# Kernel tuning notes

Measured on AMD Instinct MI355X. Metric: run time of the kernel, lower is better.

The kernel has to match this reference:

```python
import jax, jax.numpy as jnp
import numpy as np

B, N, M, K = 8, 9225, 4096, 32
D = 2          # coordinate dim
HID = 64       # MLP hidden
DOUT = 16      # MLP output / f_y channels


def setup_inputs() -> dict:
    key = jax.random.key(0)
    ks = jax.random.split(key, 10)
    y = jax.random.uniform(ks[0], (B, N, D), dtype=jnp.float32)
    x = jax.random.uniform(ks[1], (B, M, D), dtype=jnp.float32)
    f_y = jax.random.uniform(ks[2], (B, N, DOUT), dtype=jnp.float32)
    weights = jax.random.uniform(ks[3], (B, N), dtype=jnp.float32)
    neighbors_index = jax.random.randint(ks[4], (B, M, K), 0, N, dtype=jnp.int64)
    drop = jax.random.uniform(ks[5], (B, M, K)) < 0.1
    neighbors_index = jnp.where(drop, jnp.int64(-1), neighbors_index)
    # LinearChannelMLP params: 4 -> 64 -> 16, gelu between
    W1 = jax.random.normal(ks[6], (2 * D, HID), dtype=jnp.float32) * (1.0 / np.sqrt(2 * D))
    b1 = jnp.zeros((HID,), dtype=jnp.float32)
    W2 = jax.random.normal(ks[7], (HID, DOUT), dtype=jnp.float32) * (1.0 / np.sqrt(HID))
    b2 = jnp.zeros((DOUT,), dtype=jnp.float32)
    return {"y": y, "x": x, "f_y": f_y, "weights": weights,
            "W1": W1, "b1": b1, "W2": W2, "b2": b2,
            "neighbors_index": neighbors_index}


def _batched_gather(table, idx):
    # table: [B, N, ...], idx: [B, M, K] -> [B, M, K, ...]
    return jax.vmap(lambda t, i: t[i])(table, idx)


def reference(y, x, f_y, weights, W1, b1, W2, b2, neighbors_index):
    idx = jnp.where(neighbors_index == -1, 0, neighbors_index)      # [B,M,K]
    valid = (neighbors_index != -1).astype(y.dtype)[..., None]      # [B,M,K,1]

    rep_y = _batched_gather(y, idx)                                 # [B,M,K,D]
    in_f = _batched_gather(f_y, idx)                                # [B,M,K,DOUT]
    self_x = jnp.broadcast_to(x[:, :, None, :], rep_y.shape)        # [B,M,K,D]

    agg = jnp.concatenate([rep_y, self_x], axis=-1)                 # [B,M,K,2D]
    h = jax.nn.gelu(agg @ W1 + b1, approximate=False)               # [B,M,K,HID]
    kval = h @ W2 + b2                                              # [B,M,K,DOUT]

    kval = kval * in_f                                              # linear transform: k(x,y)*f(y)
    w_nbr = _batched_gather(weights, idx)[..., None]                # [B,M,K,1]
    kval = kval * w_nbr * valid
    return kval.sum(axis=2)                                         # [B,M,DOUT]
```

## Files before the change

kernel.cpp:

```cpp
#include <hip/hip_runtime.h>
#include <hip/hip_bf16.h>

#define B_    8
#define N_    9225
#define M_    4096
#define K_    32
#define HID_  64
#define DOUT_ 16

typedef __attribute__((ext_vector_type(8))) short short8;
typedef __attribute__((ext_vector_type(4))) float floatx4;
typedef __attribute__((ext_vector_type(2))) float f32x2;

static __device__ __forceinline__ short f2bf(float f) {
    __hip_bfloat16 h = __float2bfloat16(f);
    return __builtin_bit_cast(short, h);
}
static __device__ __forceinline__ float bf2f(short s) {
    unsigned u = ((unsigned)(unsigned short)s) << 16;
    return __builtin_bit_cast(float, u);
}
static __device__ __forceinline__ f32x2 splat2(float v) { return (f32x2){v, v}; }

static __device__ __forceinline__ float row16_sum(float v) {
    int t;
    t = __builtin_amdgcn_update_dpp(0, __builtin_bit_cast(int, v), 0x111, 0xF, 0xF, true);
    v += __builtin_bit_cast(float, t);
    t = __builtin_amdgcn_update_dpp(0, __builtin_bit_cast(int, v), 0x112, 0xF, 0xF, true);
    v += __builtin_bit_cast(float, t);
    t = __builtin_amdgcn_update_dpp(0, __builtin_bit_cast(int, v), 0x114, 0xF, 0xF, true);
    v += __builtin_bit_cast(float, t);
    t = __builtin_amdgcn_update_dpp(0, __builtin_bit_cast(int, v), 0x118, 0xF, 0xF, true);
    v += __builtin_bit_cast(float, t);
    return v;
}

static __device__ __forceinline__ f32x2 gelu2(f32x2 x) {
    const f32x2 xsq = x * x;
    const f32x2 t   = __builtin_elementwise_fma(xsq, splat2(0.035677408f), splat2(0.79788456f));
    const f32x2 z   = x * t;
    const f32x2 u   = z * z;
    const f32x2 a   = u + splat2(105.0f);
    const f32x2 nin = __builtin_elementwise_fma(u, a, splat2(945.0f));
    const f32x2 num = z * nin;
    const f32x2 bq  = __builtin_elementwise_fma(u, splat2(15.0f), splat2(420.0f));
    const f32x2 den = __builtin_elementwise_fma(u, bq, splat2(945.0f));
    const f32x2 r   = { __builtin_amdgcn_rcpf(den[0]), __builtin_amdgcn_rcpf(den[1]) };
    f32x2 th = num * r;
    th = __builtin_elementwise_min(__builtin_elementwise_max(th, splat2(-1.0f)), splat2(1.0f));
    const f32x2 hx = x * splat2(0.5f);
    return __builtin_elementwise_fma(hx, th, hx);
}

__global__ __launch_bounds__(256, 4) void it_kernel(
    const float* __restrict__ y,
    const float* __restrict__ x,
    const float* __restrict__ f_y,
    const float* __restrict__ weights,
    const float* __restrict__ W1,
    const float* __restrict__ b1,
    const float* __restrict__ W2,
    const float* __restrict__ b2,
    const int*   __restrict__ nbr,
    float*       __restrict__ out)
{
    __shared__ float b1L[64];
    __shared__ float b2L[16];

    const int tid = threadIdx.x;
    if (tid < 64) b1L[tid] = b1[tid];
    if (tid < 16) b2L[tid] = b2[tid];

    const int lane = tid & 63;
    const int q    = lane >> 4;
    const int nlo  = lane & 15;

    const int blk   = blockIdx.x;
    const int batch = blk & 7;
    const int pblk  = blk >> 3;
    const int wid   = tid >> 6;
    const int row0  = __builtin_amdgcn_readfirstlane(batch * M_ + pblk * 16 + wid * 4);
    const int bbase = batch * N_;

    short8 w1h[4];
    #pragma unroll
    for (int t = 0; t < 4; ++t) {
        #pragma unroll
        for (int jj = 0; jj < 8; ++jj) w1h[t][jj] = 0;
        #pragma unroll
        for (int jj = 0; jj < 4; ++jj) {
            const float wv = W1[jj * HID_ + t * 16 + nlo];
            w1h[t][jj] = (q == 0) ? f2bf(wv) : (short)0;
        }
    }

    short8 w2f[2];
    #pragma unroll
    for (int ch = 0; ch < 2; ++ch)
        #pragma unroll
        for (int jj = 0; jj < 8; ++jj) {
            const int H = (ch * 2 + (jj >> 2)) * 16 + q * 4 + (jj & 3);
            w2f[ch][jj] = f2bf(W2[H * DOUT_ + nlo]);
        }

    short xh[8], xl[8];
    #pragma unroll
    for (int it = 0; it < 4; ++it) {
        const float2 xv = *(const float2*)(x + (size_t)(row0 + it) * 2);
        const short h0 = f2bf(xv.x); const short l0 = f2bf(xv.x - bf2f(h0));
        const short h1 = f2bf(xv.y); const short l1 = f2bf(xv.y - bf2f(h1));
        xh[it * 2] = h0; xh[it * 2 + 1] = h1;
        xl[it * 2] = l0; xl[it * 2 + 1] = l1;
    }

    int raw[8];
    #pragma unroll
    for (int ph = 0; ph < 8; ++ph) {
        const int it = ph >> 1, h = ph & 1;
        raw[ph] = nbr[(size_t)(row0 + it) * K_ + h * 16 + nlo];
    }

    float2 yv[8]; float sw[8]; floatx4 fv[8];
    #define GATH(P) { \
        const int rv  = raw[P]; \
        const int vld = rv >= 0; \
        const int bn  = bbase + (vld ? rv : 0); \
        yv[P] = *(const float2*)(y + (size_t)bn * 2); \
        const float wv_ = weights[bn]; \
        sw[P] = vld ? wv_ : 0.0f; \
        fv[P] = *(const floatx4*)(f_y + (size_t)bn * DOUT_ + q * 4); \
    }
    GATH(0); GATH(1);

    __syncthreads();

    float partial[4] = {0.f, 0.f, 0.f, 0.f};
    #pragma unroll
    for (int ph = 0; ph < 8; ++ph) {
        if (ph + 2 < 8) GATH(ph + 2);
        const int it = ph >> 1;

        const float y0 = yv[ph].x, y1 = yv[ph].y;
        const short yh0 = f2bf(y0); const short yl0 = f2bf(y0 - bf2f(yh0));
        const short yh1 = f2bf(y1); const short yl1 = f2bf(y1 - bf2f(yh1));
        const bool q0 = (q == 0);
        const short z = 0;
        const short8 bhi = { q0 ? yh0 : z, q0 ? yh1 : z,
                             q0 ? xh[it * 2] : z, q0 ? xh[it * 2 + 1] : z,
                             z, z, z, z };
        const short8 blo = { q0 ? yl0 : z, q0 ? yl1 : z,
                             q0 ? xl[it * 2] : z, q0 ? xl[it * 2 + 1] : z,
                             z, z, z, z };

        floatx4 a1[4];
        #pragma unroll
        for (int t = 0; t < 4; ++t) {
            a1[t] = *(const floatx4*)&b1L[t * 16 + q * 4];
            a1[t] = __builtin_amdgcn_mfma_f32_16x16x32_bf16(w1h[t], bhi, a1[t], 0, 0, 0);
            a1[t] = __builtin_amdgcn_mfma_f32_16x16x32_bf16(w1h[t], blo, a1[t], 0, 0, 0);
        }

        short hv[16];
        #pragma unroll
        for (int t = 0; t < 4; ++t) {
            const f32x2 g01 = gelu2((f32x2){a1[t][0], a1[t][1]});
            const f32x2 g23 = gelu2((f32x2){a1[t][2], a1[t][3]});
            hv[t * 4 + 0] = f2bf(g01[0]); hv[t * 4 + 1] = f2bf(g01[1]);
            hv[t * 4 + 2] = f2bf(g23[0]); hv[t * 4 + 3] = f2bf(g23[1]);
        }
        const short8 hf0 = {hv[0], hv[1], hv[2],  hv[3],  hv[4],  hv[5],  hv[6],  hv[7]};
        const short8 hf1 = {hv[8], hv[9], hv[10], hv[11], hv[12], hv[13], hv[14], hv[15]};

        floatx4 acc = *(const floatx4*)&b2L[q * 4];
        acc = __builtin_amdgcn_mfma_f32_16x16x32_bf16(w2f[0], hf0, acc, 0, 0, 0);
        acc = __builtin_amdgcn_mfma_f32_16x16x32_bf16(w2f[1], hf1, acc, 0, 0, 0);

        const floatx4 fvp = fv[ph];
        const float   s   = sw[ph];
        #pragma unroll
        for (int r = 0; r < 4; ++r)
            partial[r] = fmaf(acc[r], fvp[r] * s, partial[r]);

        if (ph & 1) {
            #pragma unroll
            for (int r = 0; r < 4; ++r) partial[r] = row16_sum(partial[r]);
            if (nlo == 15) {
                floatx4 o = {partial[0], partial[1], partial[2], partial[3]};
                *(floatx4*)(out + (size_t)(row0 + it) * DOUT_ + q * 4) = o;
            }
            #pragma unroll
            for (int r = 0; r < 4; ++r) partial[r] = 0.f;
        }
    }
    #undef GATH
}

extern "C" void kernel_launch(void* const* d_in, const int* in_sizes, int n_in,
                              void* d_out, int out_size, void* d_ws, size_t ws_size,
                              hipStream_t stream) {
    const float* y   = (const float*)d_in[0];
    const float* x   = (const float*)d_in[1];
    const float* f_y = (const float*)d_in[2];
    const float* w   = (const float*)d_in[3];
    const float* W1  = (const float*)d_in[4];
    const float* b1  = (const float*)d_in[5];
    const float* W2  = (const float*)d_in[6];
    const float* b2  = (const float*)d_in[7];
    const int*   nbr = (const int*)d_in[8];
    float* out = (float*)d_out;

    dim3 grid(B_ * M_ / 16), block(256);
    hipLaunchKernelGGL(it_kernel, grid, block, 0, stream,
                       y, x, f_y, w, W1, b1, W2, b2, nbr, out);
}
```

Measured before the change: 108.7 us.

## Halve rows per wave, merge hi/lo MFMAs, use exp-based GELU, raise occupancy

Each wave now handles 2 output rows instead of 4, the grid doubles, and launch bounds rise to 6 blocks per CU. The goal is more parallelism and shorter per-wave critical paths for the latency-bound gather. The hi and lo bf16 parts of the input are packed into one 8-wide B operand, with W1 duplicated across both halves, so each first-layer tile takes one MFMA instead of two. The Padé tanh in GELU is replaced with an exp2 plus reciprocal formulation evaluated per scalar, trading the packed-math polynomial for transcendental instructions. This gives less pipelined gather prefetch per wave and different rounding behaviour in GELU.

```diff
diff --git a/kernel.cpp b/kernel.cpp
--- a/kernel.cpp
+++ b/kernel.cpp
@@ -10,7 +10,6 @@
 
 typedef __attribute__((ext_vector_type(8))) short short8;
 typedef __attribute__((ext_vector_type(4))) float floatx4;
-typedef __attribute__((ext_vector_type(2))) float f32x2;
 
 static __device__ __forceinline__ short f2bf(float f) {
     __hip_bfloat16 h = __float2bfloat16(f);
@@ -20,7 +19,6 @@
     unsigned u = ((unsigned)(unsigned short)s) << 16;
     return __builtin_bit_cast(float, u);
 }
-static __device__ __forceinline__ f32x2 splat2(float v) { return (f32x2){v, v}; }
 
 static __device__ __forceinline__ float row16_sum(float v) {
     int t;
@@ -35,24 +33,16 @@
     return v;
 }
 
-static __device__ __forceinline__ f32x2 gelu2(f32x2 x) {
-    const f32x2 xsq = x * x;
-    const f32x2 t   = __builtin_elementwise_fma(xsq, splat2(0.035677408f), splat2(0.79788456f));
-    const f32x2 z   = x * t;
-    const f32x2 u   = z * z;
-    const f32x2 a   = u + splat2(105.0f);
-    const f32x2 nin = __builtin_elementwise_fma(u, a, splat2(945.0f));
-    const f32x2 num = z * nin;
-    const f32x2 bq  = __builtin_elementwise_fma(u, splat2(15.0f), splat2(420.0f));
-    const f32x2 den = __builtin_elementwise_fma(u, bq, splat2(945.0f));
-    const f32x2 r   = { __builtin_amdgcn_rcpf(den[0]), __builtin_amdgcn_rcpf(den[1]) };
-    f32x2 th = num * r;
-    th = __builtin_elementwise_min(__builtin_elementwise_max(th, splat2(-1.0f)), splat2(1.0f));
-    const f32x2 hx = x * splat2(0.5f);
-    return __builtin_elementwise_fma(hx, th, hx);
+static __device__ __forceinline__ float gelu1(float x) {
+    const float z  = x * __builtin_fmaf(0.035677408f, x * x, 0.79788456f);
+    const float e  = __builtin_amdgcn_exp2f(z * 2.885390081777927f);
+    const float r  = __builtin_amdgcn_rcpf(1.0f + e);
+    const float th = __builtin_fmaf(-2.0f, r, 1.0f);
+    const float hx = 0.5f * x;
+    return __builtin_fmaf(hx, th, hx);
 }
 
-__global__ __launch_bounds__(256, 4) void it_kernel(
+__global__ __launch_bounds__(256, 6) void it_kernel(
     const float* __restrict__ y,
     const float* __restrict__ x,
     const float* __restrict__ f_y,
@@ -74,23 +64,24 @@
     const int lane = tid & 63;
     const int q    = lane >> 4;
     const int nlo  = lane & 15;
+    const bool q0  = (q == 0);
 
     const int blk   = blockIdx.x;
     const int batch = blk & 7;
     const int pblk  = blk >> 3;
     const int wid   = tid >> 6;
-    const int row0  = __builtin_amdgcn_readfirstlane(batch * M_ + pblk * 16 + wid * 4);
+    const int row0  = __builtin_amdgcn_readfirstlane(batch * M_ + pblk * 8 + wid * 2);
     const int bbase = batch * N_;
 
     short8 w1h[4];
     #pragma unroll
     for (int t = 0; t < 4; ++t) {
         #pragma unroll
-        for (int jj = 0; jj < 8; ++jj) w1h[t][jj] = 0;
-        #pragma unroll
         for (int jj = 0; jj < 4; ++jj) {
             const float wv = W1[jj * HID_ + t * 16 + nlo];
-            w1h[t][jj] = (q == 0) ? f2bf(wv) : (short)0;
+            const short b  = q0 ? f2bf(wv) : (short)0;
+            w1h[t][jj]     = b;
+            w1h[t][jj + 4] = b;
         }
     }
 
@@ -103,9 +94,9 @@
             w2f[ch][jj] = f2bf(W2[H * DOUT_ + nlo]);
         }
 
-    short xh[8], xl[8];
+    short xh[4], xl[4];
     #pragma unroll
-    for (int it = 0; it < 4; ++it) {
+    for (int it = 0; it < 2; ++it) {
         const float2 xv = *(const float2*)(x + (size_t)(row0 + it) * 2);
         const short h0 = f2bf(xv.x); const short l0 = f2bf(xv.x - bf2f(h0));
         const short h1 = f2bf(xv.y); const short l1 = f2bf(xv.y - bf2f(h1));
@@ -113,14 +104,14 @@
         xl[it * 2] = l0; xl[it * 2 + 1] = l1;
     }
 
-    int raw[8];
+    int raw[4];
     #pragma unroll
-    for (int ph = 0; ph < 8; ++ph) {
+    for (int ph = 0; ph < 4; ++ph) {
         const int it = ph >> 1, h = ph & 1;
         raw[ph] = nbr[(size_t)(row0 + it) * K_ + h * 16 + nlo];
     }
 
-    float2 yv[8]; float sw[8]; floatx4 fv[8];
+    float2 yv[4]; float sw[4]; floatx4 fv[4];
     #define GATH(P) { \
         const int rv  = raw[P]; \
         const int vld = rv >= 0; \
@@ -136,37 +127,30 @@
 
     float partial[4] = {0.f, 0.f, 0.f, 0.f};
     #pragma unroll
-    for (int ph = 0; ph < 8; ++ph) {
-        if (ph + 2 < 8) GATH(ph + 2);
+    for (int ph = 0; ph < 4; ++ph) {
+        if (ph + 2 < 4) GATH(ph + 2);
         const int it = ph >> 1;
 
         const float y0 = yv[ph].x, y1 = yv[ph].y;
         const short yh0 = f2bf(y0); const short yl0 = f2bf(y0 - bf2f(yh0));
         const short yh1 = f2bf(y1); const short yl1 = f2bf(y1 - bf2f(yh1));
-        const bool q0 = (q == 0);
-        const short z = 0;
-        const short8 bhi = { q0 ? yh0 : z, q0 ? yh1 : z,
-                             q0 ? xh[it * 2] : z, q0 ? xh[it * 2 + 1] : z,
-                             z, z, z, z };
-        const short8 blo = { q0 ? yl0 : z, q0 ? yl1 : z,
-                             q0 ? xl[it * 2] : z, q0 ? xl[it * 2 + 1] : z,
-                             z, z, z, z };
+        const short8 bfull = { yh0, yh1, xh[it * 2], xh[it * 2 + 1],
+                               yl0, yl1, xl[it * 2], xl[it * 2 + 1] };
 
         floatx4 a1[4];
         #pragma unroll
         for (int t = 0; t < 4; ++t) {
             a1[t] = *(const floatx4*)&b1L[t * 16 + q * 4];
-            a1[t] = __builtin_amdgcn_mfma_f32_16x16x32_bf16(w1h[t], bhi, a1[t], 0, 0, 0);
-            a1[t] = __builtin_amdgcn_mfma_f32_16x16x32_bf16(w1h[t], blo, a1[t], 0, 0, 0);
+            a1[t] = __builtin_amdgcn_mfma_f32_16x16x32_bf16(w1h[t], bfull, a1[t], 0, 0, 0);
         }
 
         short hv[16];
         #pragma unroll
         for (int t = 0; t < 4; ++t) {
-            const f32x2 g01 = gelu2((f32x2){a1[t][0], a1[t][1]});
-            const f32x2 g23 = gelu2((f32x2){a1[t][2], a1[t][3]});
-            hv[t * 4 + 0] = f2bf(g01[0]); hv[t * 4 + 1] = f2bf(g01[1]);
-            hv[t * 4 + 2] = f2bf(g23[0]); hv[t * 4 + 3] = f2bf(g23[1]);
+            hv[t * 4 + 0] = f2bf(gelu1(a1[t][0]));
+            hv[t * 4 + 1] = f2bf(gelu1(a1[t][1]));
+            hv[t * 4 + 2] = f2bf(gelu1(a1[t][2]));
+            hv[t * 4 + 3] = f2bf(gelu1(a1[t][3]));
         }
         const short8 hf0 = {hv[0], hv[1], hv[2],  hv[3],  hv[4],  hv[5],  hv[6],  hv[7]};
         const short8 hf1 = {hv[8], hv[9], hv[10], hv[11], hv[12], hv[13], hv[14], hv[15]};
@@ -209,7 +193,7 @@
     const int*   nbr = (const int*)d_in[8];
     float* out = (float*)d_out;
 
-    dim3 grid(B_ * M_ / 16), block(256);
+    dim3 grid(B_ * M_ / 8), block(256);
     hipLaunchKernelGGL(it_kernel, grid, block, 0, stream,
                        y, x, f_y, w, W1, b1, W2, b2, nbr, out);
 }
```

After: 110.6 us. No clear change (+1.8%).
